# Optimization experiments

Measured on AMD Instinct MI355X. Metric: run time of the kernel, lower is better.

Reference implementation:

```python
import jax, jax.numpy as jnp
import numpy as np

BC = 48
DIM = 192


def setup_inputs() -> dict:
    key = jax.random.key(0)
    ks = jax.random.split(key, 10)
    s = 0.05
    return {
        "input": jax.random.normal(ks[0], (1, BC, DIM, DIM), jnp.float32),
        "qw": jax.random.normal(ks[1], (BC // 3, BC), jnp.float32) * s,
        "qb": jax.random.normal(ks[2], (BC // 3,), jnp.float32) * s,
        "kw": jax.random.normal(ks[3], (BC // 3, BC), jnp.float32) * s,
        "kb": jax.random.normal(ks[4], (BC // 3,), jnp.float32) * s,
        "vw": jax.random.normal(ks[5], (BC, BC), jnp.float32) * s,
        "vb": jax.random.normal(ks[6], (BC,), jnp.float32) * s,
        "gamma": jnp.float32(0.1),  # torch init is 0.0; nonzero to exercise attn path
        "dw": jax.random.normal(ks[7], (BC, BC, 4, 4), jnp.float32) * s,  # torch ConvTranspose2d [in,out,kh,kw]
        "db": jax.random.normal(ks[8], (BC,), jnp.float32) * s,
    }


def reference(input, qw, qb, kw, kb, vw, vb, gamma, dw, db):
    B, C, H, W = input.shape  # B == 1
    x = input.reshape(B, C, H // 2, 2, W // 2, 2).mean(axis=(3, 5))
    h, w = H // 2, W // 2
    n = h * w
    f = x.reshape(1, C, n)
    # 1x1 Conv1d == per-position linear over channels
    q = jnp.einsum('oc,bcn->bno', qw, f) + qb            # [1, N, bc//3]
    k = jnp.einsum('oc,bcn->bon', kw, f) + kb[:, None]    # [1, bc//3, N]
    v = jnp.einsum('oc,bcn->bon', vw, f) + vb[:, None]    # [1, bc, N]
    qk = jnp.einsum('bno,bom->bnm', q, k)                 # [1, N, N]
    attn = jax.nn.softmax(qk, axis=1)                     # softmax over QUERY axis (dim 1), as in source
    o = jnp.einsum('bcn,bnm->bcm', v, attn)               # [1, bc, N]
    out = gamma * o.reshape(x.shape) + x
    # ConvTranspose2d(k=4, s=2, p=1): conv with lhs_dilation=2, pad k-1-p=2, flipped kernel
    kern = jnp.flip(jnp.transpose(dw, (1, 0, 2, 3)), axis=(2, 3))  # [out, in, kh, kw]
    y = jax.lax.conv_general_dilated(
        out, kern, window_strides=(1, 1), padding=((2, 2), (2, 2)),
        lhs_dilation=(2, 2), dimension_numbers=('NCHW', 'OIHW', 'NCHW'))
    return y + db[None, :, None, None]
```

## Files before the change

### kernel.cpp

```cpp
#include <hip/hip_runtime.h>
#include <hip/hip_bf16.h>

#define C 48
#define HH 192
#define WW 192
#define HP 96
#define WP 96
#define NP 9216

#define OFF_QB    0
#define OFF_KB    36864
#define OFF_VT2   73728
#define OFF_XT    368640
#define OFF_XTP   811008
#define OFF_WB    1118336
#define OFF_PART  1142912
#define WS_NEED_BYTES ((size_t)10580096 * 4)

typedef __attribute__((ext_vector_type(4))) short s16x4;
typedef __attribute__((ext_vector_type(8))) short s16x8;
typedef __attribute__((ext_vector_type(4))) float f32x4;

#if __has_builtin(__builtin_amdgcn_mfma_f32_16x16x16bf16_1k)
static __device__ inline f32x4 mfma16(s16x4 a, s16x4 b, f32x4 c) {
    return __builtin_amdgcn_mfma_f32_16x16x16bf16_1k(a, b, c, 0, 0, 0);
}
#else
static __device__ inline f32x4 mfma16(s16x4 a, s16x4 b, f32x4 c) {
    asm volatile("v_mfma_f32_16x16x16_bf16 %0, %1, %2, %0" : "+v"(c) : "v"(a), "v"(b));
    return c;
}
#endif

static __device__ inline f32x4 mfma32(s16x8 a, s16x8 b, f32x4 c) {
    return __builtin_amdgcn_mfma_f32_16x16x32_bf16(a, b, c, 0, 0, 0);
}

static __device__ inline float fexp2(float x) {
    float r;
    asm("v_exp_f32 %0, %1" : "=v"(r) : "v"(x));
    return r;
}

static __device__ inline unsigned short f2bf(float f) {
    union { float f; unsigned u; } v; v.f = f;
    unsigned r = v.u + 0x7fff + ((v.u >> 16) & 1);
    return (unsigned short)(r >> 16);
}

static __device__ inline float bf2f(unsigned short u) {
    union { unsigned u; float f; } v; v.u = ((unsigned)u) << 16; return v.f;
}

static __device__ inline s16x4 pack_bf16x4(float a, float b, float c, float d) {
    __hip_bfloat162 h0 = __float22bfloat162_rn(make_float2(a, b));
    __hip_bfloat162 h1 = __float22bfloat162_rn(make_float2(c, d));
    union { unsigned u[2]; s16x4 v; } pu;
    pu.u[0] = *reinterpret_cast<unsigned*>(&h0);
    pu.u[1] = *reinterpret_cast<unsigned*>(&h1);
    return pu.v;
}

__global__ void pool_k(const float* __restrict__ in, float* __restrict__ xT) {
    int idx = blockIdx.x * 256 + threadIdx.x;
    if (idx >= C * NP) return;
    int c = idx / NP, r = idx % NP;
    int y = r / WP, xx = r % WP;
    const float* p = in + (size_t)c * HH * WW + (2 * y) * WW + 2 * xx;
    xT[(size_t)r * 48 + c] = 0.25f * (p[0] + p[1] + p[WW] + p[WW + 1]);
}

__global__ void qkvprep_k(const float* __restrict__ xT,
                          const float* __restrict__ qw, const float* __restrict__ qb,
                          const float* __restrict__ kw, const float* __restrict__ kb,
                          const float* __restrict__ vw, const float* __restrict__ vb,
                          unsigned short* __restrict__ QB, unsigned short* __restrict__ KB,
                          unsigned short* __restrict__ VT2) {
    int tid = blockIdx.x * 256 + threadIdx.x;
    int p = tid % NP;
    int g = tid / NP;
    float f[C];
#pragma unroll
    for (int c4 = 0; c4 < C; c4 += 4) {
        f32x4 v = *(const f32x4*)(xT + (size_t)p * 48 + c4);
        f[c4] = v[0]; f[c4 + 1] = v[1]; f[c4 + 2] = v[2]; f[c4 + 3] = v[3];
    }
    int nt = p >> 4, nn = p & 15;
    if (g == 0) {
#pragma unroll
        for (int o = 0; o < 16; ++o) {
            float a = qb[o];
#pragma unroll
            for (int c = 0; c < C; ++c) a += qw[o * C + c] * f[c];
            QB[p * 16 + o] = f2bf(a);
        }
    } else if (g == 1) {
        const float L2E = 1.4426950408889634f;
#pragma unroll
        for (int o = 0; o < 16; ++o) {
            float a = kb[o];
#pragma unroll
            for (int c = 0; c < C; ++c) a += kw[o * C + c] * f[c];
            KB[p * 16 + o] = f2bf(a * L2E);
        }
        VT2[(size_t)nt * 1024 + 48 * 16 + nn] = 0x3F80;
#pragma unroll
        for (int r = 49; r < 64; ++r) VT2[(size_t)nt * 1024 + r * 16 + nn] = 0;
    } else {
        int c0 = (g - 2) * 16;
#pragma unroll
        for (int oo = 0; oo < 16; ++oo) {
            int o = c0 + oo;
            float a = vb[o];
#pragma unroll
            for (int c = 0; c < C; ++c) a += vw[o * C + c] * f[c];
            VT2[(size_t)nt * 1024 + o * 16 + nn] = f2bf(a);
        }
    }
}

#define MBLKS 72
#define NSPL  32
#define NSTEP 18

static __device__ __forceinline__ void attn_core32(const unsigned short* __restrict__ QB,
                                                   const unsigned short* __restrict__ VT2,
                                                   s16x4 bq0, s16x4 bq1, int n0, int lo, int hi,
                                                   f32x4 o0[4], f32x4 o1[4]) {
    const unsigned short* qp = QB + (size_t)(n0 + lo) * 16 + 4 * hi;
    const unsigned short* vp = VT2 + (size_t)(n0 >> 4) * 1024 + lo * 16 + 4 * hi;
    s16x4 aq  = *(const s16x4*)qp;
    s16x4 bv0 = *(const s16x4*)(vp);
    s16x4 bv1 = *(const s16x4*)(vp + 256);
    s16x4 bv2 = *(const s16x4*)(vp + 512);
    s16x4 bv3 = *(const s16x4*)(vp + 768);
    for (int s = 0; s < NSTEP; ++s) {
        qp += 256;
        vp += 1024;
        s16x4 aqn  = *(const s16x4*)qp;
        s16x4 bvn0 = *(const s16x4*)(vp);
        s16x4 bvn1 = *(const s16x4*)(vp + 256);
        s16x4 bvn2 = *(const s16x4*)(vp + 512);
        s16x4 bvn3 = *(const s16x4*)(vp + 768);
        f32x4 z = {0.f, 0.f, 0.f, 0.f};
        f32x4 t0 = mfma16(aq, bq0, z);
        f32x4 t1 = mfma16(aq, bq1, z);
        s16x4 p0 = pack_bf16x4(fexp2(t0[0]), fexp2(t0[1]), fexp2(t0[2]), fexp2(t0[3]));
        s16x4 p1 = pack_bf16x4(fexp2(t1[0]), fexp2(t1[1]), fexp2(t1[2]), fexp2(t1[3]));
        o0[0] = mfma16(p0, bv0, o0[0]);
        o0[1] = mfma16(p0, bv1, o0[1]);
        o0[2] = mfma16(p0, bv2, o0[2]);
        o0[3] = mfma16(p0, bv3, o0[3]);
        o1[0] = mfma16(p1, bv0, o1[0]);
        o1[1] = mfma16(p1, bv1, o1[1]);
        o1[2] = mfma16(p1, bv2, o1[2]);
        o1[3] = mfma16(p1, bv3, o1[3]);
        aq = aqn; bv0 = bvn0; bv1 = bvn1; bv2 = bvn2; bv3 = bvn3;
    }
}

__global__ __launch_bounds__(256) void attn_k(const unsigned short* __restrict__ QB,
                                              const unsigned short* __restrict__ KB,
                                              const unsigned short* __restrict__ VT2,
                                              unsigned short* __restrict__ PART) {
    const int lane = threadIdx.x & 63;
    const int lo = lane & 15, hi = lane >> 4;
    const int wv = threadIdx.x >> 6;
    const int mblk = blockIdx.x % MBLKS;
    const int nspl = blockIdx.x / MBLKS;
    const int mt0 = mblk * 128 + wv * 32;

    const s16x4 bq0 = *(const s16x4*)(KB + (size_t)(mt0 + lo) * 16 + 4 * hi);
    const s16x4 bq1 = *(const s16x4*)(KB + (size_t)(mt0 + 16 + lo) * 16 + 4 * hi);

    f32x4 o0[4], o1[4];
#pragma unroll
    for (int i = 0; i < 4; ++i) {
        o0[i] = (f32x4){0.f, 0.f, 0.f, 0.f};
        o1[i] = (f32x4){0.f, 0.f, 0.f, 0.f};
    }
    attn_core32(QB, VT2, bq0, bq1, nspl * (NP / NSPL), lo, hi, o0, o1);

    unsigned short* cp = PART + ((size_t)(mblk * 4 + wv) * NSPL + nspl) * 2048;
#pragma unroll
    for (int q = 0; q < 8; ++q) {
        const f32x4& o = (q >> 2) ? o1[q & 3] : o0[q & 3];
        s16x4 pk = pack_bf16x4(o[0], o[1], o[2], o[3]);
        *(s16x4*)(cp + q * 256 + lane * 4) = pk;
    }
}

__global__ __launch_bounds__(256) void reduce_epi_k(const unsigned short* __restrict__ PART,
                                                    const float* __restrict__ xT,
                                                    const float* __restrict__ gamma,
                                                    unsigned short* __restrict__ XTP) {
    __shared__ float sden[32];
    const int T = blockIdx.x;
    const int mt0 = (T >> 2) * 128 + (T & 3) * 32;
    const unsigned short* base = PART + (size_t)T * NSPL * 2048;
    const int t = threadIdx.x;

    if (t < 8) {
        int h = t >> 2, hi = t & 3;
        int idx = (h * 4 + 3) * 256 + (hi * 16) * 4;
        float a0 = 0.f, a1 = 0.f, a2 = 0.f, a3 = 0.f;
        for (int ns = 0; ns < NSPL; ++ns) {
            s16x4 v = *(const s16x4*)(base + ns * 2048 + idx);
            a0 += bf2f((unsigned short)v[0]);
            a1 += bf2f((unsigned short)v[1]);
            a2 += bf2f((unsigned short)v[2]);
            a3 += bf2f((unsigned short)v[3]);
        }
        sden[h * 16 + hi * 4 + 0] = a0;
        sden[h * 16 + hi * 4 + 1] = a1;
        sden[h * 16 + hi * 4 + 2] = a2;
        sden[h * 16 + hi * 4 + 3] = a3;
    }
    __syncthreads();

    float gam = gamma[0];
#pragma unroll
    for (int g = t; g < 512; g += 256) {
        int q = g >> 6, lane = g & 63;
        int h = q >> 2, ct = q & 3;
        int hi = lane >> 4, lo = lane & 15;
        int c = ct * 16 + lo;
        int idx = q * 256 + lane * 4;
        float a0 = 0.f, a1 = 0.f, a2 = 0.f, a3 = 0.f;
        for (int ns = 0; ns < NSPL; ++ns) {
            s16x4 v = *(const s16x4*)(base + ns * 2048 + idx);
            a0 += bf2f((unsigned short)v[0]);
            a1 += bf2f((unsigned short)v[1]);
            a2 += bf2f((unsigned short)v[2]);
            a3 += bf2f((unsigned short)v[3]);
        }
        if (c < 48) {
            float av[4] = {a0, a1, a2, a3};
#pragma unroll
            for (int j = 0; j < 4; ++j) {
                int ml = h * 16 + hi * 4 + j;
                int m = mt0 + ml;
                float val = gam * av[j] / sden[ml] + xT[(size_t)m * 48 + c];
                int iy = m / WP, ix = m % WP;
                XTP[((size_t)(iy + 1) * 98 + ix + 1) * 64 + c] = f2bf(val);
            }
        }
    }
}

__global__ __launch_bounds__(256) void attn_atomic_k(const unsigned short* __restrict__ QB,
                                                     const unsigned short* __restrict__ KB,
                                                     const unsigned short* __restrict__ VT2,
                                                     float* __restrict__ O4) {
    const int lane = threadIdx.x & 63;
    const int lo = lane & 15, hi = lane >> 4;
    const int wv = threadIdx.x >> 6;
    const int mblk = blockIdx.x % 72;
    const int nspl = blockIdx.x / 72;
    const int mt0 = mblk * 128 + wv * 32;
    const s16x4 bq0 = *(const s16x4*)(KB + (size_t)(mt0 + lo) * 16 + 4 * hi);
    const s16x4 bq1 = *(const s16x4*)(KB + (size_t)(mt0 + 16 + lo) * 16 + 4 * hi);
    f32x4 o0[4], o1[4];
#pragma unroll
    for (int i = 0; i < 4; ++i) {
        o0[i] = (f32x4){0.f, 0.f, 0.f, 0.f};
        o1[i] = (f32x4){0.f, 0.f, 0.f, 0.f};
    }
    attn_core32(QB, VT2, bq0, bq1, nspl * 288, lo, hi, o0, o1);
    float* Oc = O4 + (size_t)(nspl & 3) * (NP * 64);
#pragma unroll
    for (int ct = 0; ct < 4; ++ct)
#pragma unroll
        for (int j = 0; j < 4; ++j) {
            atomicAdd(&Oc[(size_t)(mt0 + 4 * hi + j) * 64 + 16 * ct + lo], o0[ct][j]);
            atomicAdd(&Oc[(size_t)(mt0 + 16 + 4 * hi + j) * 64 + 16 * ct + lo], o1[ct][j]);
        }
}

__global__ void epi_atomic_k(const float* __restrict__ O4, const float* __restrict__ xT,
                             const float* __restrict__ gamma, unsigned short* __restrict__ XTP) {
    int m = blockIdx.x * 256 + threadIdx.x;
    if (m >= NP) return;
    int iy = m / WP, ix = m % WP;
    unsigned short* xp = XTP + ((size_t)(iy + 1) * 98 + ix + 1) * 64;
    float den = 0.f;
#pragma unroll
    for (int cp = 0; cp < 4; ++cp) den += O4[(size_t)cp * (NP * 64) + (size_t)m * 64 + 48];
    float rg = gamma[0] / den;
#pragma unroll
    for (int c = 0; c < C; ++c) {
        float o = 0.f;
#pragma unroll
        for (int cp = 0; cp < 4; ++cp) o += O4[(size_t)cp * (NP * 64) + (size_t)m * 64 + c];
        xp[c] = f2bf(rg * o + xT[(size_t)m * 48 + c]);
    }
}

__global__ void wprep_k(const float* __restrict__ dw, unsigned short* __restrict__ WB,
                        unsigned short* __restrict__ XTP) {
    int idx = blockIdx.x * 256 + threadIdx.x;
    if (idx < 3104) {
        int pos = idx >> 3, cc = (idx & 7) * 8;
        int row, col;
        if (pos < 98)       { row = 0;             col = pos; }
        else if (pos < 196) { row = 97;            col = pos - 98; }
        else if (pos < 292) { row = pos - 196 + 1; col = 0; }
        else                { row = pos - 292 + 1; col = 97; }
        s16x8 zz = (s16x8){0, 0, 0, 0, 0, 0, 0, 0};
        *(s16x8*)(XTP + ((size_t)row * 98 + col) * 64 + cc) = zz;
    }
    if (idx >= 16 * 48 * 64) return;
    int ci = idx & 63;
    int co = (idx >> 6) % 48;
    int kidx = idx / (48 * 64);
    float v = (ci < C) ? dw[((size_t)ci * C + co) * 16 + kidx] : 0.f;
    WB[idx] = f2bf(v);
}

__global__ __launch_bounds__(128) void convt_mfma_k(const unsigned short* __restrict__ XTP,
                                                    const unsigned short* __restrict__ WB,
                                                    const float* __restrict__ db,
                                                    float* __restrict__ y) {
    const int lane = threadIdx.x & 63;
    const int lo = lane & 15, hi = lane >> 4;
    const int wv = threadIdx.x >> 6;
    const int b = blockIdx.x;
    const int i3 = b % 3;
    const int r3 = b / 3;
    const int px = r3 & 1;
    const int py = (r3 >> 1) & 1;
    const int oyp = r3 >> 2;

    const int sy[2] = {0, py ? 1 : -1};
    const int kyt[2] = {py ? 2 : 1, py ? 0 : 3};
    const int sx[2] = {0, px ? 1 : -1};
    const int kxt[2] = {px ? 2 : 1, px ? 0 : 3};

    s16x8 bw[2][2][2][3];
#pragma unroll
    for (int ty = 0; ty < 2; ++ty)
#pragma unroll
        for (int tx = 0; tx < 2; ++tx) {
            const unsigned short* wp = WB + (size_t)(kyt[ty] * 4 + kxt[tx]) * 48 * 64;
#pragma unroll
            for (int kk = 0; kk < 2; ++kk)
#pragma unroll
                for (int ct = 0; ct < 3; ++ct)
                    bw[ty][tx][kk][ct] = *(const s16x8*)(wp + (size_t)(ct * 16 + lo) * 64 + kk * 32 + 8 * hi);
        }
    float bias[3];
#pragma unroll
    for (int ct = 0; ct < 3; ++ct) bias[ct] = db[ct * 16 + lo];

    const int oy = 2 * oyp + py;
    const int ox0 = (wv * 3 + i3) * 16;
    f32x4 acc[3];
#pragma unroll
    for (int ct = 0; ct < 3; ++ct) acc[ct] = (f32x4){bias[ct], bias[ct], bias[ct], bias[ct]};
#pragma unroll
    for (int ty = 0; ty < 2; ++ty) {
        int R0 = (oyp + sy[ty] + 1) * 98;
#pragma unroll
        for (int tx = 0; tx < 2; ++tx) {
            const unsigned short* ap = XTP + (size_t)(R0 + ox0 + sx[tx] + 1 + lo) * 64 + 8 * hi;
#pragma unroll
            for (int kk = 0; kk < 2; ++kk) {
                s16x8 a = *(const s16x8*)(ap + kk * 32);
                acc[0] = mfma32(a, bw[ty][tx][kk][0], acc[0]);
                acc[1] = mfma32(a, bw[ty][tx][kk][1], acc[1]);
                acc[2] = mfma32(a, bw[ty][tx][kk][2], acc[2]);
            }
        }
    }
#pragma unroll
    for (int ct = 0; ct < 3; ++ct)
#pragma unroll
        for (int j = 0; j < 4; ++j)
            y[(size_t)(ct * 16 + lo) * (HH * WW) + oy * WW + 2 * (ox0 + 4 * hi + j) + px] = acc[ct][j];
}

extern "C" void kernel_launch(void* const* d_in, const int* in_sizes, int n_in,
                              void* d_out, int out_size, void* d_ws, size_t ws_size,
                              hipStream_t stream) {
    const float* in    = (const float*)d_in[0];
    const float* qw    = (const float*)d_in[1];
    const float* qb    = (const float*)d_in[2];
    const float* kw    = (const float*)d_in[3];
    const float* kb    = (const float*)d_in[4];
    const float* vw    = (const float*)d_in[5];
    const float* vb    = (const float*)d_in[6];
    const float* gamma = (const float*)d_in[7];
    const float* dw    = (const float*)d_in[8];
    const float* db    = (const float*)d_in[9];
    float* out = (float*)d_out;

    float* ws = (float*)d_ws;
    unsigned short* QB   = (unsigned short*)(ws + OFF_QB);
    unsigned short* KB   = (unsigned short*)(ws + OFF_KB);
    unsigned short* VT2  = (unsigned short*)(ws + OFF_VT2);
    float*          xT   = ws + OFF_XT;
    unsigned short* XTP  = (unsigned short*)(ws + OFF_XTP);
    unsigned short* WB   = (unsigned short*)(ws + OFF_WB);
    unsigned short* PART = (unsigned short*)(ws + OFF_PART);

    pool_k<<<(C * NP + 255) / 256, 256, 0, stream>>>(in, xT);
    qkvprep_k<<<(5 * NP) / 256, 256, 0, stream>>>(xT, qw, qb, kw, kb, vw, vb, QB, KB, VT2);
    wprep_k<<<(16 * 48 * 64) / 256, 256, 0, stream>>>(dw, WB, XTP);

    if (ws_size >= WS_NEED_BYTES) {
        attn_k<<<MBLKS * NSPL, 256, 0, stream>>>(QB, KB, VT2, PART);
        reduce_epi_k<<<288, 256, 0, stream>>>(PART, xT, gamma, XTP);
    } else {
        float* O4 = (float*)PART;
        hipMemsetAsync(O4, 0, (size_t)4 * NP * 64 * sizeof(float), stream);
        attn_atomic_k<<<72 * 32, 256, 0, stream>>>(QB, KB, VT2, O4);
        epi_atomic_k<<<(NP + 255) / 256, 256, 0, stream>>>(O4, xT, gamma, XTP);
    }
    convt_mfma_k<<<96 * 2 * 2 * 3, 128, 0, stream>>>(XTP, WB, db, out);
}
```

Before: 86.53 us.

## Merge pool and weight prep kernels, widen qkv prep and reduce parallelism

Fuses the pooling and deconvolution weight-prep kernels into one launch to save a kernel launch. Restructures the QKV projection so each thread computes a single output channel (96 threads per position) instead of 16 outputs per thread, which raises parallelism but makes every thread reload its 48 input channels. Splits the reduction epilogue over twice as many blocks, one half-tile each, at the cost of recomputing the denominators in both blocks.

```diff
diff --git a/kernel.cpp b/kernel.cpp
--- a/kernel.cpp
+++ b/kernel.cpp
@@ -61,13 +61,34 @@
     return pu.v;
 }
 
-__global__ void pool_k(const float* __restrict__ in, float* __restrict__ xT) {
-    int idx = blockIdx.x * 256 + threadIdx.x;
-    if (idx >= C * NP) return;
-    int c = idx / NP, r = idx % NP;
-    int y = r / WP, xx = r % WP;
-    const float* p = in + (size_t)c * HH * WW + (2 * y) * WW + 2 * xx;
-    xT[(size_t)r * 48 + c] = 0.25f * (p[0] + p[1] + p[WW] + p[WW + 1]);
+__global__ void pool_wprep_k(const float* __restrict__ in, float* __restrict__ xT,
+                             const float* __restrict__ dw, unsigned short* __restrict__ WB,
+                             unsigned short* __restrict__ XTP) {
+    int b = blockIdx.x;
+    if (b < 1728) {
+        int idx = b * 256 + threadIdx.x;
+        int c = idx / NP, r = idx % NP;
+        int y = r / WP, xx = r % WP;
+        const float* p = in + (size_t)c * HH * WW + (2 * y) * WW + 2 * xx;
+        xT[(size_t)r * 48 + c] = 0.25f * (p[0] + p[1] + p[WW] + p[WW + 1]);
+        return;
+    }
+    int idx = (b - 1728) * 256 + threadIdx.x;
+    if (idx < 3104) {
+        int pos = idx >> 3, cc = (idx & 7) * 8;
+        int row, col;
+        if (pos < 98)       { row = 0;             col = pos; }
+        else if (pos < 196) { row = 97;            col = pos - 98; }
+        else if (pos < 292) { row = pos - 196 + 1; col = 0; }
+        else                { row = pos - 292 + 1; col = 97; }
+        s16x8 zz = (s16x8){0, 0, 0, 0, 0, 0, 0, 0};
+        *(s16x8*)(XTP + ((size_t)row * 98 + col) * 64 + cc) = zz;
+    }
+    int ci = idx & 63;
+    int co = (idx >> 6) % 48;
+    int kidx = idx / (48 * 64);
+    float v = (ci < C) ? dw[((size_t)ci * C + co) * 16 + kidx] : 0.f;
+    WB[idx] = f2bf(v);
 }
 
 __global__ void qkvprep_k(const float* __restrict__ xT,
@@ -77,45 +98,36 @@
                           unsigned short* __restrict__ QB, unsigned short* __restrict__ KB,
                           unsigned short* __restrict__ VT2) {
     int tid = blockIdx.x * 256 + threadIdx.x;
-    int p = tid % NP;
-    int g = tid / NP;
+    int p = tid / 96, o = tid % 96;
+    int nt = p >> 4, nn = p & 15;
+    if (o >= 80) {
+        VT2[(size_t)nt * 1024 + (o - 32) * 16 + nn] = (o == 80) ? 0x3F80 : 0;
+        return;
+    }
     float f[C];
 #pragma unroll
     for (int c4 = 0; c4 < C; c4 += 4) {
         f32x4 v = *(const f32x4*)(xT + (size_t)p * 48 + c4);
         f[c4] = v[0]; f[c4 + 1] = v[1]; f[c4 + 2] = v[2]; f[c4 + 3] = v[3];
     }
-    int nt = p >> 4, nn = p & 15;
-    if (g == 0) {
-#pragma unroll
-        for (int o = 0; o < 16; ++o) {
-            float a = qb[o];
-#pragma unroll
-            for (int c = 0; c < C; ++c) a += qw[o * C + c] * f[c];
-            QB[p * 16 + o] = f2bf(a);
-        }
-    } else if (g == 1) {
+    if (o < 16) {
+        float a = qb[o];
+#pragma unroll
+        for (int c = 0; c < C; ++c) a += qw[o * C + c] * f[c];
+        QB[p * 16 + o] = f2bf(a);
+    } else if (o < 32) {
+        int oo = o - 16;
         const float L2E = 1.4426950408889634f;
-#pragma unroll
-        for (int o = 0; o < 16; ++o) {
-            float a = kb[o];
-#pragma unroll
-            for (int c = 0; c < C; ++c) a += kw[o * C + c] * f[c];
-            KB[p * 16 + o] = f2bf(a * L2E);
-        }
-        VT2[(size_t)nt * 1024 + 48 * 16 + nn] = 0x3F80;
-#pragma unroll
-        for (int r = 49; r < 64; ++r) VT2[(size_t)nt * 1024 + r * 16 + nn] = 0;
+        float a = kb[oo];
+#pragma unroll
+        for (int c = 0; c < C; ++c) a += kw[oo * C + c] * f[c];
+        KB[p * 16 + oo] = f2bf(a * L2E);
     } else {
-        int c0 = (g - 2) * 16;
-#pragma unroll
-        for (int oo = 0; oo < 16; ++oo) {
-            int o = c0 + oo;
-            float a = vb[o];
-#pragma unroll
-            for (int c = 0; c < C; ++c) a += vw[o * C + c] * f[c];
-            VT2[(size_t)nt * 1024 + o * 16 + nn] = f2bf(a);
-        }
+        int vo = o - 32;
+        float a = vb[vo];
+#pragma unroll
+        for (int c = 0; c < C; ++c) a += vw[vo * C + c] * f[c];
+        VT2[(size_t)nt * 1024 + vo * 16 + nn] = f2bf(a);
     }
 }
 
@@ -195,7 +207,8 @@
                                                     const float* __restrict__ gamma,
                                                     unsigned short* __restrict__ XTP) {
     __shared__ float sden[32];
-    const int T = blockIdx.x;
+    const int B = blockIdx.x;
+    const int T = B >> 1, half = B & 1;
     const int mt0 = (T >> 2) * 128 + (T & 3) * 32;
     const unsigned short* base = PART + (size_t)T * NSPL * 2048;
     const int t = threadIdx.x;
@@ -219,31 +232,29 @@
     __syncthreads();
 
     float gam = gamma[0];
-#pragma unroll
-    for (int g = t; g < 512; g += 256) {
-        int q = g >> 6, lane = g & 63;
-        int h = q >> 2, ct = q & 3;
-        int hi = lane >> 4, lo = lane & 15;
-        int c = ct * 16 + lo;
-        int idx = q * 256 + lane * 4;
-        float a0 = 0.f, a1 = 0.f, a2 = 0.f, a3 = 0.f;
-        for (int ns = 0; ns < NSPL; ++ns) {
-            s16x4 v = *(const s16x4*)(base + ns * 2048 + idx);
-            a0 += bf2f((unsigned short)v[0]);
-            a1 += bf2f((unsigned short)v[1]);
-            a2 += bf2f((unsigned short)v[2]);
-            a3 += bf2f((unsigned short)v[3]);
-        }
-        if (c < 48) {
-            float av[4] = {a0, a1, a2, a3};
-#pragma unroll
-            for (int j = 0; j < 4; ++j) {
-                int ml = h * 16 + hi * 4 + j;
-                int m = mt0 + ml;
-                float val = gam * av[j] / sden[ml] + xT[(size_t)m * 48 + c];
-                int iy = m / WP, ix = m % WP;
-                XTP[((size_t)(iy + 1) * 98 + ix + 1) * 64 + c] = f2bf(val);
-            }
+    int g = half * 256 + t;
+    int q = g >> 6, lane = g & 63;
+    int h = q >> 2, ct = q & 3;
+    int hi = lane >> 4, lo = lane & 15;
+    int c = ct * 16 + lo;
+    int idx = q * 256 + lane * 4;
+    float a0 = 0.f, a1 = 0.f, a2 = 0.f, a3 = 0.f;
+    for (int ns = 0; ns < NSPL; ++ns) {
+        s16x4 v = *(const s16x4*)(base + ns * 2048 + idx);
+        a0 += bf2f((unsigned short)v[0]);
+        a1 += bf2f((unsigned short)v[1]);
+        a2 += bf2f((unsigned short)v[2]);
+        a3 += bf2f((unsigned short)v[3]);
+    }
+    if (c < 48) {
+        float av[4] = {a0, a1, a2, a3};
+#pragma unroll
+        for (int j = 0; j < 4; ++j) {
+            int ml = h * 16 + hi * 4 + j;
+            int m = mt0 + ml;
+            float val = gam * av[j] / sden[ml] + xT[(size_t)m * 48 + c];
+            int iy = m / WP, ix = m % WP;
+            XTP[((size_t)(iy + 1) * 98 + ix + 1) * 64 + c] = f2bf(val);
         }
     }
 }
@@ -294,27 +305,6 @@
         for (int cp = 0; cp < 4; ++cp) o += O4[(size_t)cp * (NP * 64) + (size_t)m * 64 + c];
         xp[c] = f2bf(rg * o + xT[(size_t)m * 48 + c]);
     }
-}
-
-__global__ void wprep_k(const float* __restrict__ dw, unsigned short* __restrict__ WB,
-                        unsigned short* __restrict__ XTP) {
-    int idx = blockIdx.x * 256 + threadIdx.x;
-    if (idx < 3104) {
-        int pos = idx >> 3, cc = (idx & 7) * 8;
-        int row, col;
-        if (pos < 98)       { row = 0;             col = pos; }
-        else if (pos < 196) { row = 97;            col = pos - 98; }
-        else if (pos < 292) { row = pos - 196 + 1; col = 0; }
-        else                { row = pos - 292 + 1; col = 97; }
-        s16x8 zz = (s16x8){0, 0, 0, 0, 0, 0, 0, 0};
-        *(s16x8*)(XTP + ((size_t)row * 98 + col) * 64 + cc) = zz;
-    }
-    if (idx >= 16 * 48 * 64) return;
-    int ci = idx & 63;
-    int co = (idx >> 6) % 48;
-    int kidx = idx / (48 * 64);
-    float v = (ci < C) ? dw[((size_t)ci * C + co) * 16 + kidx] : 0.f;
-    WB[idx] = f2bf(v);
 }
 
 __global__ __launch_bounds__(128) void convt_mfma_k(const unsigned short* __restrict__ XTP,
@@ -403,13 +393,12 @@
     unsigned short* WB   = (unsigned short*)(ws + OFF_WB);
     unsigned short* PART = (unsigned short*)(ws + OFF_PART);
 
-    pool_k<<<(C * NP + 255) / 256, 256, 0, stream>>>(in, xT);
-    qkvprep_k<<<(5 * NP) / 256, 256, 0, stream>>>(xT, qw, qb, kw, kb, vw, vb, QB, KB, VT2);
-    wprep_k<<<(16 * 48 * 64) / 256, 256, 0, stream>>>(dw, WB, XTP);
+    pool_wprep_k<<<1920, 256, 0, stream>>>(in, xT, dw, WB, XTP);
+    qkvprep_k<<<3456, 256, 0, stream>>>(xT, qw, qb, kw, kb, vw, vb, QB, KB, VT2);
 
     if (ws_size >= WS_NEED_BYTES) {
         attn_k<<<MBLKS * NSPL, 256, 0, stream>>>(QB, KB, VT2, PART);
-        reduce_epi_k<<<288, 256, 0, stream>>>(PART, xT, gamma, XTP);
+        reduce_epi_k<<<576, 256, 0, stream>>>(PART, xT, gamma, XTP);
     } else {
         float* O4 = (float*)PART;
         hipMemsetAsync(O4, 0, (size_t)4 * NP * 64 * sizeof(float), stream);
```

Result: slower. 90.93 us (+5.1%).

## Deepen attention load prefetch to two stages and halve the key-axis split count

Applied to the files above, without the earlier changes.

The attention inner loop now keeps two steps of Q/V fragments in flight instead of one, to hide more global-load latency behind the MFMA and exp work. The split of the summation axis drops from 32 to 16 chunks of 36 steps each. This halves the partial buffers written and later reduced, and shrinks the workspace. The QB region is enlarged so the extra prefetch reads past the end stay in bounds, and launch bounds now request two blocks per CU. In exchange the grid has half as many blocks, each doing more serial work, and register pressure rises.

```diff
diff --git a/kernel.cpp b/kernel.cpp
--- a/kernel.cpp
+++ b/kernel.cpp
@@ -9,13 +9,13 @@
 #define NP 9216
 
 #define OFF_QB    0
-#define OFF_KB    36864
-#define OFF_VT2   73728
-#define OFF_XT    368640
-#define OFF_XTP   811008
-#define OFF_WB    1118336
-#define OFF_PART  1142912
-#define WS_NEED_BYTES ((size_t)10580096 * 4)
+#define OFF_KB    73728
+#define OFF_VT2   147456
+#define OFF_XT    442368
+#define OFF_XTP   884736
+#define OFF_WB    1192064
+#define OFF_PART  1216640
+#define WS_NEED_BYTES ((size_t)5935232 * 4)
 
 typedef __attribute__((ext_vector_type(4))) short s16x4;
 typedef __attribute__((ext_vector_type(8))) short s16x8;
@@ -120,49 +120,59 @@
 }
 
 #define MBLKS 72
-#define NSPL  32
-#define NSTEP 18
-
+#define NSPL  16
+#define NSTEP 36
+
+template<int STEPS>
 static __device__ __forceinline__ void attn_core32(const unsigned short* __restrict__ QB,
                                                    const unsigned short* __restrict__ VT2,
                                                    s16x4 bq0, s16x4 bq1, int n0, int lo, int hi,
                                                    f32x4 o0[4], f32x4 o1[4]) {
     const unsigned short* qp = QB + (size_t)(n0 + lo) * 16 + 4 * hi;
     const unsigned short* vp = VT2 + (size_t)(n0 >> 4) * 1024 + lo * 16 + 4 * hi;
-    s16x4 aq  = *(const s16x4*)qp;
-    s16x4 bv0 = *(const s16x4*)(vp);
-    s16x4 bv1 = *(const s16x4*)(vp + 256);
-    s16x4 bv2 = *(const s16x4*)(vp + 512);
-    s16x4 bv3 = *(const s16x4*)(vp + 768);
-    for (int s = 0; s < NSTEP; ++s) {
-        qp += 256;
-        vp += 1024;
+    s16x4 aqA  = *(const s16x4*)qp;
+    s16x4 bvA0 = *(const s16x4*)(vp);
+    s16x4 bvA1 = *(const s16x4*)(vp + 256);
+    s16x4 bvA2 = *(const s16x4*)(vp + 512);
+    s16x4 bvA3 = *(const s16x4*)(vp + 768);
+    qp += 256; vp += 1024;
+    s16x4 aqB  = *(const s16x4*)qp;
+    s16x4 bvB0 = *(const s16x4*)(vp);
+    s16x4 bvB1 = *(const s16x4*)(vp + 256);
+    s16x4 bvB2 = *(const s16x4*)(vp + 512);
+    s16x4 bvB3 = *(const s16x4*)(vp + 768);
+
+    for (int s = 0; s < STEPS; ++s) {
+        qp += 256; vp += 1024;
         s16x4 aqn  = *(const s16x4*)qp;
         s16x4 bvn0 = *(const s16x4*)(vp);
         s16x4 bvn1 = *(const s16x4*)(vp + 256);
         s16x4 bvn2 = *(const s16x4*)(vp + 512);
         s16x4 bvn3 = *(const s16x4*)(vp + 768);
+
         f32x4 z = {0.f, 0.f, 0.f, 0.f};
-        f32x4 t0 = mfma16(aq, bq0, z);
-        f32x4 t1 = mfma16(aq, bq1, z);
+        f32x4 t0 = mfma16(aqA, bq0, z);
+        f32x4 t1 = mfma16(aqA, bq1, z);
         s16x4 p0 = pack_bf16x4(fexp2(t0[0]), fexp2(t0[1]), fexp2(t0[2]), fexp2(t0[3]));
         s16x4 p1 = pack_bf16x4(fexp2(t1[0]), fexp2(t1[1]), fexp2(t1[2]), fexp2(t1[3]));
-        o0[0] = mfma16(p0, bv0, o0[0]);
-        o0[1] = mfma16(p0, bv1, o0[1]);
-        o0[2] = mfma16(p0, bv2, o0[2]);
-        o0[3] = mfma16(p0, bv3, o0[3]);
-        o1[0] = mfma16(p1, bv0, o1[0]);
-        o1[1] = mfma16(p1, bv1, o1[1]);
-        o1[2] = mfma16(p1, bv2, o1[2]);
-        o1[3] = mfma16(p1, bv3, o1[3]);
-        aq = aqn; bv0 = bvn0; bv1 = bvn1; bv2 = bvn2; bv3 = bvn3;
-    }
-}
-
-__global__ __launch_bounds__(256) void attn_k(const unsigned short* __restrict__ QB,
-                                              const unsigned short* __restrict__ KB,
-                                              const unsigned short* __restrict__ VT2,
-                                              unsigned short* __restrict__ PART) {
+        o0[0] = mfma16(p0, bvA0, o0[0]);
+        o0[1] = mfma16(p0, bvA1, o0[1]);
+        o0[2] = mfma16(p0, bvA2, o0[2]);
+        o0[3] = mfma16(p0, bvA3, o0[3]);
+        o1[0] = mfma16(p1, bvA0, o1[0]);
+        o1[1] = mfma16(p1, bvA1, o1[1]);
+        o1[2] = mfma16(p1, bvA2, o1[2]);
+        o1[3] = mfma16(p1, bvA3, o1[3]);
+
+        aqA = aqB; bvA0 = bvB0; bvA1 = bvB1; bvA2 = bvB2; bvA3 = bvB3;
+        aqB = aqn; bvB0 = bvn0; bvB1 = bvn1; bvB2 = bvn2; bvB3 = bvn3;
+    }
+}
+
+__global__ __launch_bounds__(256, 2) void attn_k(const unsigned short* __restrict__ QB,
+                                                 const unsigned short* __restrict__ KB,
+                                                 const unsigned short* __restrict__ VT2,
+                                                 unsigned short* __restrict__ PART) {
     const int lane = threadIdx.x & 63;
     const int lo = lane & 15, hi = lane >> 4;
     const int wv = threadIdx.x >> 6;
@@ -179,7 +189,7 @@
         o0[i] = (f32x4){0.f, 0.f, 0.f, 0.f};
         o1[i] = (f32x4){0.f, 0.f, 0.f, 0.f};
     }
-    attn_core32(QB, VT2, bq0, bq1, nspl * (NP / NSPL), lo, hi, o0, o1);
+    attn_core32<NSTEP>(QB, VT2, bq0, bq1, nspl * (NP / NSPL), lo, hi, o0, o1);
 
     unsigned short* cp = PART + ((size_t)(mblk * 4 + wv) * NSPL + nspl) * 2048;
 #pragma unroll
@@ -266,7 +276,7 @@
         o0[i] = (f32x4){0.f, 0.f, 0.f, 0.f};
         o1[i] = (f32x4){0.f, 0.f, 0.f, 0.f};
     }
-    attn_core32(QB, VT2, bq0, bq1, nspl * 288, lo, hi, o0, o1);
+    attn_core32<18>(QB, VT2, bq0, bq1, nspl * 288, lo, hi, o0, o1);
     float* Oc = O4 + (size_t)(nspl & 3) * (NP * 64);
 #pragma unroll
     for (int ct = 0; ct < 4; ++ct)
```

After: 84.76 us. 2.0% less time.
